# Kernel tuning notes

Hardware: AMD Instinct MI355X
Metric: run time of the kernel (lower is better)

## Reference

```python
import jax, jax.numpy as jnp
import numpy as np
import math

N = 50000
E = 600000
HID = 128
NG = 50
NF = 128
CUTOFF = 10.0
OFFSET = 0.0


def ssp(x):
    # shifted softplus, standard SchNet activation
    return jax.nn.softplus(x) - jnp.log(2.0).astype(x.dtype)


def setup_inputs() -> dict:
    key = jax.random.key(0)
    ks = jax.random.split(key, 12)
    x = jax.random.normal(ks[0], (N, HID), dtype=jnp.float32)
    ji_pairs = jax.random.randint(ks[1], (2, E), 0, N, dtype=jnp.int64)
    e_ji = jax.random.uniform(ks[2], (E,), dtype=jnp.float32) * CUTOFF
    e_ji_basis = jax.random.normal(ks[3], (E, NG), dtype=jnp.float32)
    # filter_nn: Linear(NG, NF) -> ssp -> Linear(NF, NF)
    fw1 = jax.random.normal(ks[4], (NF, NG), dtype=jnp.float32) * (1.0 / np.sqrt(NG))
    fb1 = jnp.zeros((NF,), jnp.float32)
    fw2 = jax.random.normal(ks[5], (NF, NF), dtype=jnp.float32) * (1.0 / np.sqrt(NF))
    fb2 = jnp.zeros((NF,), jnp.float32)
    # CFConv linear1 (no bias), linear2
    w1 = jax.random.normal(ks[6], (NF, HID), dtype=jnp.float32) * (1.0 / np.sqrt(HID))
    w2 = jax.random.normal(ks[7], (HID, NF), dtype=jnp.float32) * (1.0 / np.sqrt(NF))
    b2 = jnp.zeros((HID,), jnp.float32)
    # InteractionBlock linear3
    w3 = jax.random.normal(ks[8], (HID, HID), dtype=jnp.float32) * (1.0 / np.sqrt(HID))
    b3 = jnp.zeros((HID,), jnp.float32)
    return {"x": x, "ji_pairs": ji_pairs, "e_ji": e_ji, "e_ji_basis": e_ji_basis,
            "fw1": fw1, "fb1": fb1, "fw2": fw2, "fb2": fb2,
            "w1": w1, "w2": w2, "b2": b2, "w3": w3, "b3": b3}


def reference(x, ji_pairs, e_ji, e_ji_basis, fw1, fb1, fw2, fb2, w1, w2, b2, w3, b3):
    # cosine cutoff  [E]
    C = 0.25 * (jnp.cos((e_ji - OFFSET) * (np.pi / (CUTOFF - OFFSET))) + 1.0)
    # filter MLP on edge basis  [E, NF]
    h = ssp(e_ji_basis @ fw1.T + fb1)
    W = (h @ fw2.T + fb2) * C[:, None]
    # node projection  [N, NF]
    xh = x @ w1.T
    # gather x_j, modulate by W, scatter-add to target nodes (PyG source_to_target)
    src, dst = ji_pairs[0], ji_pairs[1]
    msg = xh[src] * W                                # [E, NF]
    agg = jax.ops.segment_sum(msg, dst, num_segments=N)  # [N, NF]
    out = agg @ w2.T + b2                            # [N, HID]
    out = ssp(out)
    out = out @ w3.T + b3
    return out
```

## Files before the change

kernel.cpp:

```cpp
#include <hip/hip_runtime.h>

typedef float f32x4 __attribute__((ext_vector_type(4)));
typedef short bf16x8 __attribute__((ext_vector_type(8)));
typedef unsigned short u16;
typedef unsigned int u32;

__device__ __forceinline__ u32 cvt_pk_bf16(float lo, float hi) {
    u32 r;
    asm("v_cvt_pk_bf16_f32 %0, %1, %2" : "=v"(r) : "v"(lo), "v"(hi));
    return r;
}

__device__ __forceinline__ u16 f2b(float f) {
    union { float f; u32 u; } v; v.f = f;
    u32 r = v.u + 0x7fffu + ((v.u >> 16) & 1u);
    return (u16)(r >> 16);
}
__device__ __forceinline__ float b2f_lo(u32 p) {
    union { u32 u; float f; } v; v.u = p << 16; return v.f;
}
__device__ __forceinline__ float b2f_hi(u32 p) {
    union { u32 u; float f; } v; v.u = p & 0xffff0000u; return v.f;
}

__device__ __forceinline__ float ssp(float x) {
    return fmaxf(x, 0.0f) + __logf(1.0f + __expf(-fabsf(x))) - 0.6931471805599453f;
}

__global__ void prep_weights(const float* __restrict__ fw1,
                             const float* __restrict__ fw2,
                             const float* __restrict__ w1,
                             const float* __restrict__ w2,
                             const float* __restrict__ w3,
                             u16* __restrict__ out) {
    int t = blockIdx.x * blockDim.x + threadIdx.x;
    if (t < 128 * 64) {
        int c = t >> 6, k = t & 63;
        out[t] = f2b(k < 50 ? fw1[c * 50 + k] : 0.0f);
        return;
    }
    t -= 128 * 64;
    if (t < 16384) { out[8192 + t] = f2b(fw2[t]); return; }
    t -= 16384;
    if (t < 16384) { out[8192 + 16384 + t] = f2b(w1[t]); return; }
    t -= 16384;
    if (t < 16384) { out[8192 + 32768 + t] = f2b(w2[t]); return; }
    t -= 16384;
    if (t < 16384) { out[8192 + 49152 + t] = f2b(w3[t]); return; }
}

template <int ACT, int OBF>
__global__ __launch_bounds__(256, 3) void linear128(
    const float* __restrict__ in, const u16* __restrict__ wb,
    const float* __restrict__ bias, void* __restrict__ outv, int M) {
    __shared__ u16 in_lds[64 * 136];
    __shared__ u16 w_lds[128 * 136];

    const int tid = threadIdx.x;
    const int r0 = blockIdx.x * 64;

    for (int idx = tid; idx < 128 * 16; idx += 256) {
        int c = idx >> 4, kc = (idx & 15) * 8;
        *reinterpret_cast<uint4*>(&w_lds[c * 136 + kc]) =
            *reinterpret_cast<const uint4*>(&wb[c * 128 + kc]);
    }
    for (int idx = tid; idx < 64 * 32; idx += 256) {
        int r = idx >> 5, kc = (idx & 31) * 4;
        int row = r0 + r;
        float4 v = make_float4(0.f, 0.f, 0.f, 0.f);
        if (row < M) v = *reinterpret_cast<const float4*>(&in[(size_t)row * 128 + kc]);
        u32* p = reinterpret_cast<u32*>(&in_lds[r * 136 + kc]);
        p[0] = cvt_pk_bf16(v.x, v.y); p[1] = cvt_pk_bf16(v.z, v.w);
    }
    __syncthreads();

    const int l = tid & 63, w = tid >> 6;
    const int lr = l & 15, lg = l >> 4;

    f32x4 acc[8] = {};
    for (int ks = 0; ks < 4; ++ks) {
        bf16x8 a = *reinterpret_cast<const bf16x8*>(
            &in_lds[(w * 16 + lr) * 136 + ks * 32 + lg * 8]);
        for (int n = 0; n < 8; ++n) {
            bf16x8 b = *reinterpret_cast<const bf16x8*>(
                &w_lds[(n * 16 + lr) * 136 + ks * 32 + lg * 8]);
            acc[n] = __builtin_amdgcn_mfma_f32_16x16x32_bf16(a, b, acc[n], 0, 0, 0);
        }
    }

    for (int n = 0; n < 8; ++n) {
        int c = n * 16 + lr;
        float bv = bias ? bias[c] : 0.0f;
        for (int i = 0; i < 4; ++i) {
            int row = r0 + w * 16 + lg * 4 + i;
            if (row < M) {
                float v = acc[n][i] + bv;
                if (ACT) v = ssp(v);
                if (OBF) ((u16*)outv)[(size_t)row * 128 + c] = f2b(v);
                else     ((float*)outv)[(size_t)row * 128 + c] = v;
            }
        }
    }
}

__global__ __launch_bounds__(256) void edge_mlp(
    const float* __restrict__ basis, const float* __restrict__ e_ji,
    const u16* __restrict__ fw1b, const u16* __restrict__ fw2b,
    const float* __restrict__ fb1, const float* __restrict__ fb2,
    const int* __restrict__ epos, u16* __restrict__ Wb,
    int E, int nTiles) {
    __shared__ u16 bas[2][32 * 72];
    __shared__ u16 hb[32 * 136];

    const int tid = threadIdx.x;
    const int l = tid & 63, w = tid >> 6;
    const int lr = l & 15, lg = l >> 4;
    const int c8 = lg * 8, c4 = lg * 4;

    bf16x8 wa1[2][2], wa2[2][4];
    float4 b1v[2], b2v[2];
#pragma unroll
    for (int i = 0; i < 2; ++i) {
        const u16* p1 = &fw1b[(size_t)((w * 2 + i) * 16 + lr) * 64];
#pragma unroll
        for (int ks = 0; ks < 2; ++ks)
            wa1[i][ks] = *reinterpret_cast<const bf16x8*>(p1 + ks * 32 + c8);
        const u16* p2 = &fw2b[(size_t)((w * 2 + i) * 16 + lr) * 128];
#pragma unroll
        for (int ks = 0; ks < 4; ++ks)
            wa2[i][ks] = *reinterpret_cast<const bf16x8*>(p2 + ks * 32 + c8);
        b1v[i] = *reinterpret_cast<const float4*>(&fb1[(w * 2 + i) * 16 + c4]);
        b2v[i] = *reinterpret_cast<const float4*>(&fb2[(w * 2 + i) * 16 + c4]);
    }

    for (int idx = tid; idx < 2 * 32 * 7; idx += 256) {
        int b = idx / 224, rem = idx - b * 224;
        int row = rem / 7, q = rem - row * 7;
        *reinterpret_cast<u32*>(&bas[b][row * 72 + 50 + 2 * q]) = 0u;
    }

    int srow[4], scol[4]; bool sv[4];
#pragma unroll
    for (int r = 0; r < 4; ++r) {
        int idx = tid + r * 256;
        sv[r] = idx < 800;
        int rr = idx / 25;
        srow[r] = rr; scol[r] = (idx - rr * 25) * 2;
    }

    int it = blockIdx.x;
    if (it >= nTiles) return;

    float2 stg[4];
#pragma unroll
    for (int r = 0; r < 4; ++r) {
        if (sv[r]) {
            int er = it * 32 + srow[r]; if (er >= E) er = E - 1;
            stg[r] = *reinterpret_cast<const float2*>(&basis[(size_t)er * 50 + scol[r]]);
        }
    }
#pragma unroll
    for (int r = 0; r < 4; ++r)
        if (sv[r])
            *reinterpret_cast<u32*>(&bas[0][srow[r] * 72 + scol[r]]) =
                cvt_pk_bf16(stg[r].x, stg[r].y);

    const int stride = gridDim.x;
    int buf = 0;
    for (; it < nTiles; it += stride) {
        const int nxt = it + stride;
        const bool hn = nxt < nTiles;
        float2 stg2[4];
        if (hn) {
#pragma unroll
            for (int r = 0; r < 4; ++r) {
                if (sv[r]) {
                    int er = nxt * 32 + srow[r]; if (er >= E) er = E - 1;
                    stg2[r] = *reinterpret_cast<const float2*>(
                        &basis[(size_t)er * 50 + scol[r]]);
                }
            }
        }
        const int er0 = it * 32 + lr, er1 = er0 + 16;
        const int ec0 = er0 < E ? er0 : E - 1;
        const int ec1 = er1 < E ? er1 : E - 1;
        const int ep0 = epos[ec0], ep1 = epos[ec1];
        const float ej0 = e_ji[ec0], ej1 = e_ji[ec1];

        __syncthreads();

        f32x4 acc1[2][2] = {};
#pragma unroll
        for (int ks = 0; ks < 2; ++ks) {
            bf16x8 bb0 = *reinterpret_cast<const bf16x8*>(
                &bas[buf][lr * 72 + ks * 32 + c8]);
            bf16x8 bb1 = *reinterpret_cast<const bf16x8*>(
                &bas[buf][(16 + lr) * 72 + ks * 32 + c8]);
#pragma unroll
            for (int i = 0; i < 2; ++i) {
                acc1[0][i] = __builtin_amdgcn_mfma_f32_16x16x32_bf16(wa1[i][ks], bb0, acc1[0][i], 0, 0, 0);
                acc1[1][i] = __builtin_amdgcn_mfma_f32_16x16x32_bf16(wa1[i][ks], bb1, acc1[1][i], 0, 0, 0);
            }
        }
#pragma unroll
        for (int t = 0; t < 2; ++t) {
#pragma unroll
            for (int i = 0; i < 2; ++i) {
                u32* d = reinterpret_cast<u32*>(
                    &hb[(t * 16 + lr) * 136 + (w * 2 + i) * 16 + c4]);
                d[0] = cvt_pk_bf16(ssp(acc1[t][i][0] + b1v[i].x),
                                   ssp(acc1[t][i][1] + b1v[i].y));
                d[1] = cvt_pk_bf16(ssp(acc1[t][i][2] + b1v[i].z),
                                   ssp(acc1[t][i][3] + b1v[i].w));
            }
        }
        __syncthreads();

        f32x4 acc2[2][2] = {};
#pragma unroll
        for (int ks = 0; ks < 4; ++ks) {
            bf16x8 hb0 = *reinterpret_cast<const bf16x8*>(
                &hb[lr * 136 + ks * 32 + c8]);
            bf16x8 hb1 = *reinterpret_cast<const bf16x8*>(
                &hb[(16 + lr) * 136 + ks * 32 + c8]);
#pragma unroll
            for (int i = 0; i < 2; ++i) {
                acc2[0][i] = __builtin_amdgcn_mfma_f32_16x16x32_bf16(wa2[i][ks], hb0, acc2[0][i], 0, 0, 0);
                acc2[1][i] = __builtin_amdgcn_mfma_f32_16x16x32_bf16(wa2[i][ks], hb1, acc2[1][i], 0, 0, 0);
            }
        }
#pragma unroll
        for (int t = 0; t < 2; ++t) {
            const int er = t == 0 ? er0 : er1;
            if (er < E) {
                const float ej = t == 0 ? ej0 : ej1;
                const int pos = t == 0 ? ep0 : ep1;
                const float cv = 0.25f * (__cosf(ej * 0.31415926535897932f) + 1.0f);
#pragma unroll
                for (int i = 0; i < 2; ++i) {
                    uint2 pk;
                    pk.x = cvt_pk_bf16((acc2[t][i][0] + b2v[i].x) * cv,
                                       (acc2[t][i][1] + b2v[i].y) * cv);
                    pk.y = cvt_pk_bf16((acc2[t][i][2] + b2v[i].z) * cv,
                                       (acc2[t][i][3] + b2v[i].w) * cv);
                    *reinterpret_cast<uint2*>(
                        &Wb[(size_t)pos * 128 + (w * 2 + i) * 16 + c4]) = pk;
                }
            }
        }
        if (hn) {
#pragma unroll
            for (int r = 0; r < 4; ++r)
                if (sv[r])
                    *reinterpret_cast<u32*>(&bas[buf ^ 1][srow[r] * 72 + scol[r]]) =
                        cvt_pk_bf16(stg2[r].x, stg2[r].y);
        }
        buf ^= 1;
    }
}

__global__ void hist_kernel(const int* __restrict__ pairs, int* __restrict__ deg, int E) {
    int e = blockIdx.x * blockDim.x + threadIdx.x;
    if (e < E) atomicAdd(&deg[pairs[E + e]], 1);
}

__global__ void scan_a(const int* __restrict__ deg, int* __restrict__ incl,
                       int* __restrict__ bsum, int N) {
    __shared__ int s[256];
    int i = blockIdx.x * 256 + threadIdx.x;
    int v = (i < N) ? deg[i] : 0;
    s[threadIdx.x] = v; __syncthreads();
    for (int off = 1; off < 256; off <<= 1) {
        int t = (threadIdx.x >= off) ? s[threadIdx.x - off] : 0;
        __syncthreads();
        s[threadIdx.x] += t; __syncthreads();
    }
    if (i < N) incl[i] = s[threadIdx.x];
    if (threadIdx.x == 255) bsum[blockIdx.x] = s[255];
}

__global__ void scan_b(int* __restrict__ bsum, int nb) {
    __shared__ int s[256];
    int v = (threadIdx.x < nb) ? bsum[threadIdx.x] : 0;
    s[threadIdx.x] = v; __syncthreads();
    for (int off = 1; off < 256; off <<= 1) {
        int t = (threadIdx.x >= off) ? s[threadIdx.x - off] : 0;
        __syncthreads();
        s[threadIdx.x] += t; __syncthreads();
    }
    if (threadIdx.x < nb) bsum[threadIdx.x] = s[threadIdx.x] - v;
}

__global__ void scan_c(const int* __restrict__ incl, const int* __restrict__ deg,
                       const int* __restrict__ bsum, int* __restrict__ rowst,
                       int* __restrict__ cursor, int N) {
    int i = blockIdx.x * 256 + threadIdx.x;
    if (i < N) {
        int r = incl[i] - deg[i] + bsum[blockIdx.x];
        rowst[i] = r; cursor[i] = r;
    }
}

__global__ void fill_kernel(const int* __restrict__ pairs, int* __restrict__ cursor,
                            int* __restrict__ esrc, int* __restrict__ epos, int E) {
    int e = blockIdx.x * blockDim.x + threadIdx.x;
    if (e < E) {
        int s = pairs[e], d = pairs[E + e];
        int pos = atomicAdd(&cursor[d], 1);
        esrc[pos] = s;
        epos[e] = pos;
    }
}

__global__ __launch_bounds__(256) void aggregate(
    const u16* __restrict__ Wb, const u16* __restrict__ xhb,
    const int* __restrict__ rowst, const int* __restrict__ deg,
    const int* __restrict__ esrc, float* __restrict__ agg, int N) {
    const int w = threadIdx.x >> 6, lane = threadIdx.x & 63;
    const int n = blockIdx.x * 4 + w;
    if (n >= N) return;
    const int rs = rowst[n], d = deg[n];
    float a0 = 0.f, a1 = 0.f;
    int s = (d > 0) ? esrc[rs] : 0;
    for (int k = 0; k < d; ++k) {
        int cur = s;
        if (k + 1 < d) s = esrc[rs + k + 1];
        u32 wp = *reinterpret_cast<const u32*>(&Wb[(size_t)(rs + k) * 128 + lane * 2]);
        u32 xp = *reinterpret_cast<const u32*>(&xhb[(size_t)cur * 128 + lane * 2]);
        a0 = fmaf(b2f_lo(xp), b2f_lo(wp), a0);
        a1 = fmaf(b2f_hi(xp), b2f_hi(wp), a1);
    }
    float2 r; r.x = a0; r.y = a1;
    *reinterpret_cast<float2*>(&agg[(size_t)n * 128 + lane * 2]) = r;
}

__global__ __launch_bounds__(256, 2) void edge_kernel(
    const float* __restrict__ basis, const float* __restrict__ e_ji,
    const int* __restrict__ pairs, const float* __restrict__ xh,
    const u16* __restrict__ fw1b, const u16* __restrict__ fw2b,
    const float* __restrict__ fb1, const float* __restrict__ fb2,
    float* __restrict__ agg, int E) {
    __shared__ u16 hb[64 * 136];
    __shared__ u16 fw1_lds[128 * 72];
    __shared__ u16 fw2_lds[128 * 136];
    __shared__ float cc[64];
    __shared__ int s_src[64];
    __shared__ int s_dst[64];

    const int tid = threadIdx.x;
    const int e0 = blockIdx.x * 64;

    for (int idx = tid; idx < 128 * 8; idx += 256) {
        int c = idx >> 3, kc = (idx & 7) * 8;
        *reinterpret_cast<uint4*>(&fw1_lds[c * 72 + kc]) =
            *reinterpret_cast<const uint4*>(&fw1b[c * 64 + kc]);
    }
    for (int idx = tid; idx < 128 * 16; idx += 256) {
        int c = idx >> 4, kc = (idx & 15) * 8;
        *reinterpret_cast<uint4*>(&fw2_lds[c * 136 + kc]) =
            *reinterpret_cast<const uint4*>(&fw2b[c * 128 + kc]);
    }
    for (int idx = tid; idx < 64 * 64; idx += 256) {
        int e = idx >> 6, k = idx & 63;
        int eg = e0 + e;
        float v = (k < 50 && eg < E) ? basis[(size_t)eg * 50 + k] : 0.0f;
        hb[e * 72 + k] = f2b(v);
    }
    if (tid < 64) {
        int eg = e0 + tid;
        if (eg < E) {
            cc[tid] = 0.25f * (__cosf(e_ji[eg] * 0.31415926535897932f) + 1.0f);
            s_src[tid] = pairs[eg];
            s_dst[tid] = pairs[E + eg];
        } else { cc[tid] = 0.0f; s_src[tid] = 0; s_dst[tid] = 0; }
    }
    __syncthreads();

    const int l = tid & 63, w = tid >> 6;
    const int lr = l & 15, lg = l >> 4;

    f32x4 acc1[8] = {};
    for (int ks = 0; ks < 2; ++ks) {
        bf16x8 a = *reinterpret_cast<const bf16x8*>(
            &hb[(w * 16 + lr) * 72 + ks * 32 + lg * 8]);
        for (int n = 0; n < 8; ++n) {
            bf16x8 b = *reinterpret_cast<const bf16x8*>(
                &fw1_lds[(n * 16 + lr) * 72 + ks * 32 + lg * 8]);
            acc1[n] = __builtin_amdgcn_mfma_f32_16x16x32_bf16(a, b, acc1[n], 0, 0, 0);
        }
    }
    __syncthreads();

    for (int n = 0; n < 8; ++n) {
        int c = n * 16 + lr;
        float bv = fb1[c];
        for (int i = 0; i < 4; ++i) {
            int r = w * 16 + lg * 4 + i;
            hb[r * 136 + c] = f2b(ssp(acc1[n][i] + bv));
        }
    }
    __syncthreads();

    f32x4 acc2[8] = {};
    for (int ks = 0; ks < 4; ++ks) {
        bf16x8 a = *reinterpret_cast<const bf16x8*>(
            &hb[(w * 16 + lr) * 136 + ks * 32 + lg * 8]);
        for (int n = 0; n < 8; ++n) {
            bf16x8 b = *reinterpret_cast<const bf16x8*>(
                &fw2_lds[(n * 16 + lr) * 136 + ks * 32 + lg * 8]);
            acc2[n] = __builtin_amdgcn_mfma_f32_16x16x32_bf16(a, b, acc2[n], 0, 0, 0);
        }
    }

    for (int n = 0; n < 8; ++n) {
        int c = n * 16 + lr;
        float bv = fb2[c];
        for (int i = 0; i < 4; ++i) {
            int eloc = w * 16 + lg * 4 + i;
            if (e0 + eloc < E) {
                float Wv = (acc2[n][i] + bv) * cc[eloc];
                float val = xh[(size_t)s_src[eloc] * 128 + c] * Wv;
                unsafeAtomicAdd(&agg[(size_t)s_dst[eloc] * 128 + c], val);
            }
        }
    }
}

extern "C" void kernel_launch(void* const* d_in, const int* in_sizes, int n_in,
                              void* d_out, int out_size, void* d_ws, size_t ws_size,
                              hipStream_t stream) {
    const float* x      = (const float*)d_in[0];
    const int*   pairs  = (const int*)d_in[1];
    const float* e_ji   = (const float*)d_in[2];
    const float* basis  = (const float*)d_in[3];
    const float* fw1    = (const float*)d_in[4];
    const float* fb1    = (const float*)d_in[5];
    const float* fw2    = (const float*)d_in[6];
    const float* fb2    = (const float*)d_in[7];
    const float* w1     = (const float*)d_in[8];
    const float* w2     = (const float*)d_in[9];
    const float* b2     = (const float*)d_in[10];
    const float* w3     = (const float*)d_in[11];
    const float* b3     = (const float*)d_in[12];
    float* out = (float*)d_out;

    const int N = in_sizes[0] / 128;
    const int E = in_sizes[2];
    const int nodeBlocks = (N + 63) / 64;
    const int nchunks = (N + 255) / 256;
    char* ws = (char*)d_ws;

    size_t off = 0;
    auto nxt = [&](size_t bytes) {
        size_t o = off; off = (off + bytes + 255) & ~(size_t)255; return o;
    };
    u16*   Wb     = (u16*)  (ws + nxt((size_t)E * 128 * 2));
    u16*   xhb    = (u16*)  (ws + nxt((size_t)N * 128 * 2));
    float* agg    = (float*)(ws + nxt((size_t)N * 128 * 4));
    u16*   wb     = (u16*)  (ws + nxt(81920 * 2));
    int*   deg    = (int*)  (ws + nxt((size_t)N * 4));
    int*   incl   = (int*)  (ws + nxt((size_t)N * 4));
    int*   rowst  = (int*)  (ws + nxt((size_t)N * 4));
    int*   cursor = (int*)  (ws + nxt((size_t)N * 4));
    int*   bsum   = (int*)  (ws + nxt(1024));
    int*   esrc   = (int*)  (ws + nxt((size_t)E * 4));
    int*   epos   = (int*)  (ws + nxt((size_t)E * 4));
    const size_t needed = off;

    const u16* fw1b = wb;
    const u16* fw2b = wb + 8192;
    const u16* w1b  = wb + 8192 + 16384;
    const u16* w2b  = wb + 8192 + 32768;
    const u16* w3b  = wb + 8192 + 49152;

    if (ws_size >= needed && nchunks <= 256) {
        prep_weights<<<288, 256, 0, stream>>>(fw1, fw2, w1, w2, w3, wb);
        hipMemsetAsync(deg, 0, (size_t)N * 4, stream);

        linear128<0, 1><<<nodeBlocks, 256, 0, stream>>>(x, w1b, nullptr, xhb, N);

        hist_kernel<<<(E + 255) / 256, 256, 0, stream>>>(pairs, deg, E);
        scan_a<<<nchunks, 256, 0, stream>>>(deg, incl, bsum, N);
        scan_b<<<1, 256, 0, stream>>>(bsum, nchunks);
        scan_c<<<nchunks, 256, 0, stream>>>(incl, deg, bsum, rowst, cursor, N);
        fill_kernel<<<(E + 255) / 256, 256, 0, stream>>>(pairs, cursor, esrc, epos, E);

        const int nTiles = (E + 31) / 32;
        const int grid = nTiles < 2048 ? nTiles : 2048;
        edge_mlp<<<grid, 256, 0, stream>>>(basis, e_ji, fw1b, fw2b,
                                           fb1, fb2, epos, Wb, E, nTiles);
        aggregate<<<(N + 3) / 4, 256, 0, stream>>>(Wb, xhb, rowst, deg,
                                                   esrc, agg, N);

        linear128<1, 0><<<nodeBlocks, 256, 0, stream>>>(agg, w2b, b2, out, N);
        linear128<0, 0><<<nodeBlocks, 256, 0, stream>>>(out, w3b, b3, out, N);
    } else {
        const size_t nodeBytes = (size_t)N * 128 * sizeof(float);
        float* xhf   = (float*)ws;
        float* aggf  = (float*)(ws + nodeBytes);
        u16*   wbf   = (u16*)(ws + 2 * nodeBytes);
        const u16* ffw1b = wbf;
        const u16* ffw2b = wbf + 8192;
        const u16* fw1bw = wbf + 8192 + 16384;
        const u16* fw2bw = wbf + 8192 + 32768;
        const u16* fw3bw = wbf + 8192 + 49152;

        prep_weights<<<288, 256, 0, stream>>>(fw1, fw2, w1, w2, w3, wbf);
        hipMemsetAsync(aggf, 0, nodeBytes, stream);
        linear128<0, 0><<<nodeBlocks, 256, 0, stream>>>(x, fw1bw, nullptr, xhf, N);
        edge_kernel<<<(E + 63) / 64, 256, 0, stream>>>(basis, e_ji, pairs, xhf,
                                                       ffw1b, ffw2b, fb1, fb2, aggf, E);
        linear128<1, 0><<<nodeBlocks, 256, 0, stream>>>(aggf, fw2bw, b2, out, N);
        linear128<0, 0><<<nodeBlocks, 256, 0, stream>>>(out, fw3bw, b3, out, N);
    }
}
```

Before: 326.5 us.

## Fuse tail linears into one kernel, double-buffer edge MLP LDS, deepen aggregate prefetch

Replaces the two node-level linear128 launches (linear2 with ssp, then linear3) with one persistent fused_tail kernel. It keeps the ssp intermediate in LDS, so the N x 128 float intermediate no longer makes a round trip through global memory. In edge_mlp it double-buffers the hidden LDS tile, drops one barrier per iteration, simplifies the basis staging map, and cuts the grid from 2048 to 1536. The aggregate loop now prefetches the next edge's Wb and xh values one step ahead to hide gather latency. The trade-off is more LDS and registers per block.

```diff
diff --git a/kernel.cpp b/kernel.cpp
--- a/kernel.cpp
+++ b/kernel.cpp
@@ -108,9 +108,9 @@
     const u16* __restrict__ fw1b, const u16* __restrict__ fw2b,
     const float* __restrict__ fb1, const float* __restrict__ fb2,
     const int* __restrict__ epos, u16* __restrict__ Wb,
-    int E, int nTiles) {
+    int E, int nTiles, int stride) {
     __shared__ u16 bas[2][32 * 72];
-    __shared__ u16 hb[32 * 136];
+    __shared__ u16 hb[2][32 * 136];
 
     const int tid = threadIdx.x;
     const int l = tid & 63, w = tid >> 6;
@@ -139,46 +139,38 @@
         *reinterpret_cast<u32*>(&bas[b][row * 72 + 50 + 2 * q]) = 0u;
     }
 
-    int srow[4], scol[4]; bool sv[4];
-#pragma unroll
-    for (int r = 0; r < 4; ++r) {
-        int idx = tid + r * 256;
-        sv[r] = idx < 800;
-        int rr = idx / 25;
-        srow[r] = rr; scol[r] = (idx - rr * 25) * 2;
-    }
+    const int srow = tid & 31, cb = tid >> 5;
 
     int it = blockIdx.x;
     if (it >= nTiles) return;
 
-    float2 stg[4];
-#pragma unroll
-    for (int r = 0; r < 4; ++r) {
-        if (sv[r]) {
-            int er = it * 32 + srow[r]; if (er >= E) er = E - 1;
-            stg[r] = *reinterpret_cast<const float2*>(&basis[(size_t)er * 50 + scol[r]]);
-        }
-    }
-#pragma unroll
-    for (int r = 0; r < 4; ++r)
-        if (sv[r])
-            *reinterpret_cast<u32*>(&bas[0][srow[r] * 72 + scol[r]]) =
-                cvt_pk_bf16(stg[r].x, stg[r].y);
-
-    const int stride = gridDim.x;
+    {
+        int er = it * 32 + srow; if (er >= E) er = E - 1;
+        const float* rp = &basis[(size_t)er * 50];
+#pragma unroll
+        for (int r = 0; r < 4; ++r) {
+            int c = cb + r * 8;
+            if (c < 25) {
+                float2 v = *reinterpret_cast<const float2*>(rp + 2 * c);
+                *reinterpret_cast<u32*>(&bas[0][srow * 72 + 2 * c]) =
+                    cvt_pk_bf16(v.x, v.y);
+            }
+        }
+    }
+    __syncthreads();
+
     int buf = 0;
-    for (; it < nTiles; it += stride) {
+    for (; it < nTiles; it += stride, buf ^= 1) {
         const int nxt = it + stride;
         const bool hn = nxt < nTiles;
-        float2 stg2[4];
+        float2 stg[4];
         if (hn) {
+            int er = nxt * 32 + srow; if (er >= E) er = E - 1;
+            const float* rp = &basis[(size_t)er * 50];
 #pragma unroll
             for (int r = 0; r < 4; ++r) {
-                if (sv[r]) {
-                    int er = nxt * 32 + srow[r]; if (er >= E) er = E - 1;
-                    stg2[r] = *reinterpret_cast<const float2*>(
-                        &basis[(size_t)er * 50 + scol[r]]);
-                }
+                int c = cb + r * 8;
+                if (c < 25) stg[r] = *reinterpret_cast<const float2*>(rp + 2 * c);
             }
         }
         const int er0 = it * 32 + lr, er1 = er0 + 16;
@@ -187,8 +179,6 @@
         const int ep0 = epos[ec0], ep1 = epos[ec1];
         const float ej0 = e_ji[ec0], ej1 = e_ji[ec1];
 
-        __syncthreads();
-
         f32x4 acc1[2][2] = {};
 #pragma unroll
         for (int ks = 0; ks < 2; ++ks) {
@@ -207,22 +197,31 @@
 #pragma unroll
             for (int i = 0; i < 2; ++i) {
                 u32* d = reinterpret_cast<u32*>(
-                    &hb[(t * 16 + lr) * 136 + (w * 2 + i) * 16 + c4]);
+                    &hb[buf][(t * 16 + lr) * 136 + (w * 2 + i) * 16 + c4]);
                 d[0] = cvt_pk_bf16(ssp(acc1[t][i][0] + b1v[i].x),
                                    ssp(acc1[t][i][1] + b1v[i].y));
                 d[1] = cvt_pk_bf16(ssp(acc1[t][i][2] + b1v[i].z),
                                    ssp(acc1[t][i][3] + b1v[i].w));
             }
         }
+        if (hn) {
+#pragma unroll
+            for (int r = 0; r < 4; ++r) {
+                int c = cb + r * 8;
+                if (c < 25)
+                    *reinterpret_cast<u32*>(&bas[buf ^ 1][srow * 72 + 2 * c]) =
+                        cvt_pk_bf16(stg[r].x, stg[r].y);
+            }
+        }
         __syncthreads();
 
         f32x4 acc2[2][2] = {};
 #pragma unroll
         for (int ks = 0; ks < 4; ++ks) {
             bf16x8 hb0 = *reinterpret_cast<const bf16x8*>(
-                &hb[lr * 136 + ks * 32 + c8]);
+                &hb[buf][lr * 136 + ks * 32 + c8]);
             bf16x8 hb1 = *reinterpret_cast<const bf16x8*>(
-                &hb[(16 + lr) * 136 + ks * 32 + c8]);
+                &hb[buf][(16 + lr) * 136 + ks * 32 + c8]);
 #pragma unroll
             for (int i = 0; i < 2; ++i) {
                 acc2[0][i] = __builtin_amdgcn_mfma_f32_16x16x32_bf16(wa2[i][ks], hb0, acc2[0][i], 0, 0, 0);
@@ -248,14 +247,130 @@
                 }
             }
         }
+    }
+}
+
+__global__ __launch_bounds__(256) void fused_tail(
+    const float* __restrict__ agg, const u16* __restrict__ w2b,
+    const u16* __restrict__ w3b, const float* __restrict__ b2,
+    const float* __restrict__ b3, float* __restrict__ out,
+    int N, int nTiles, int stride) {
+    __shared__ u16 bas[2][32 * 136];
+    __shared__ u16 hb[2][32 * 136];
+
+    const int tid = threadIdx.x;
+    const int l = tid & 63, w = tid >> 6;
+    const int lr = l & 15, lg = l >> 4;
+    const int c8 = lg * 8, c4 = lg * 4;
+
+    bf16x8 wA[2][4], wB[2][4];
+    float4 b2v[2], b3v[2];
+#pragma unroll
+    for (int i = 0; i < 2; ++i) {
+        const u16* pA = &w2b[(size_t)((w * 2 + i) * 16 + lr) * 128];
+        const u16* pB = &w3b[(size_t)((w * 2 + i) * 16 + lr) * 128];
+#pragma unroll
+        for (int ks = 0; ks < 4; ++ks) {
+            wA[i][ks] = *reinterpret_cast<const bf16x8*>(pA + ks * 32 + c8);
+            wB[i][ks] = *reinterpret_cast<const bf16x8*>(pB + ks * 32 + c8);
+        }
+        b2v[i] = *reinterpret_cast<const float4*>(&b2[(w * 2 + i) * 16 + c4]);
+        b3v[i] = *reinterpret_cast<const float4*>(&b3[(w * 2 + i) * 16 + c4]);
+    }
+
+    const int srow = tid & 31, cb = tid >> 5;
+
+    int it = blockIdx.x;
+    if (it >= nTiles) return;
+
+    {
+        int nd = it * 32 + srow; if (nd >= N) nd = N - 1;
+        const float* rp = &agg[(size_t)nd * 128];
+#pragma unroll
+        for (int r = 0; r < 8; ++r) {
+            int c = cb + r * 8;
+            float2 v = *reinterpret_cast<const float2*>(rp + 2 * c);
+            *reinterpret_cast<u32*>(&bas[0][srow * 136 + 2 * c]) =
+                cvt_pk_bf16(v.x, v.y);
+        }
+    }
+    __syncthreads();
+
+    int buf = 0;
+    for (; it < nTiles; it += stride, buf ^= 1) {
+        const int nxt = it + stride;
+        const bool hn = nxt < nTiles;
+        float2 stg[8];
         if (hn) {
-#pragma unroll
-            for (int r = 0; r < 4; ++r)
-                if (sv[r])
-                    *reinterpret_cast<u32*>(&bas[buf ^ 1][srow[r] * 72 + scol[r]]) =
-                        cvt_pk_bf16(stg2[r].x, stg2[r].y);
-        }
-        buf ^= 1;
+            int nd = nxt * 32 + srow; if (nd >= N) nd = N - 1;
+            const float* rp = &agg[(size_t)nd * 128];
+#pragma unroll
+            for (int r = 0; r < 8; ++r)
+                stg[r] = *reinterpret_cast<const float2*>(rp + 2 * (cb + r * 8));
+        }
+
+        f32x4 acc1[2][2] = {};
+#pragma unroll
+        for (int ks = 0; ks < 4; ++ks) {
+            bf16x8 bb0 = *reinterpret_cast<const bf16x8*>(
+                &bas[buf][lr * 136 + ks * 32 + c8]);
+            bf16x8 bb1 = *reinterpret_cast<const bf16x8*>(
+                &bas[buf][(16 + lr) * 136 + ks * 32 + c8]);
+#pragma unroll
+            for (int i = 0; i < 2; ++i) {
+                acc1[0][i] = __builtin_amdgcn_mfma_f32_16x16x32_bf16(wA[i][ks], bb0, acc1[0][i], 0, 0, 0);
+                acc1[1][i] = __builtin_amdgcn_mfma_f32_16x16x32_bf16(wA[i][ks], bb1, acc1[1][i], 0, 0, 0);
+            }
+        }
+#pragma unroll
+        for (int t = 0; t < 2; ++t) {
+#pragma unroll
+            for (int i = 0; i < 2; ++i) {
+                u32* d = reinterpret_cast<u32*>(
+                    &hb[buf][(t * 16 + lr) * 136 + (w * 2 + i) * 16 + c4]);
+                d[0] = cvt_pk_bf16(ssp(acc1[t][i][0] + b2v[i].x),
+                                   ssp(acc1[t][i][1] + b2v[i].y));
+                d[1] = cvt_pk_bf16(ssp(acc1[t][i][2] + b2v[i].z),
+                                   ssp(acc1[t][i][3] + b2v[i].w));
+            }
+        }
+        if (hn) {
+#pragma unroll
+            for (int r = 0; r < 8; ++r)
+                *reinterpret_cast<u32*>(&bas[buf ^ 1][srow * 136 + 2 * (cb + r * 8)]) =
+                    cvt_pk_bf16(stg[r].x, stg[r].y);
+        }
+        __syncthreads();
+
+        f32x4 acc2[2][2] = {};
+#pragma unroll
+        for (int ks = 0; ks < 4; ++ks) {
+            bf16x8 hb0 = *reinterpret_cast<const bf16x8*>(
+                &hb[buf][lr * 136 + ks * 32 + c8]);
+            bf16x8 hb1 = *reinterpret_cast<const bf16x8*>(
+                &hb[buf][(16 + lr) * 136 + ks * 32 + c8]);
+#pragma unroll
+            for (int i = 0; i < 2; ++i) {
+                acc2[0][i] = __builtin_amdgcn_mfma_f32_16x16x32_bf16(wB[i][ks], hb0, acc2[0][i], 0, 0, 0);
+                acc2[1][i] = __builtin_amdgcn_mfma_f32_16x16x32_bf16(wB[i][ks], hb1, acc2[1][i], 0, 0, 0);
+            }
+        }
+#pragma unroll
+        for (int t = 0; t < 2; ++t) {
+            int nd = it * 32 + t * 16 + lr;
+            if (nd < N) {
+#pragma unroll
+                for (int i = 0; i < 2; ++i) {
+                    float4 o;
+                    o.x = acc2[t][i][0] + b3v[i].x;
+                    o.y = acc2[t][i][1] + b3v[i].y;
+                    o.z = acc2[t][i][2] + b3v[i].z;
+                    o.w = acc2[t][i][3] + b3v[i].w;
+                    *reinterpret_cast<float4*>(
+                        &out[(size_t)nd * 128 + (w * 2 + i) * 16 + c4]) = o;
+                }
+            }
+        }
     }
 }
 
@@ -321,12 +436,20 @@
     if (n >= N) return;
     const int rs = rowst[n], d = deg[n];
     float a0 = 0.f, a1 = 0.f;
-    int s = (d > 0) ? esrc[rs] : 0;
+    int s1 = (d > 0) ? esrc[rs] : 0;
+    int s2 = (d > 1) ? esrc[rs + 1] : 0;
+    u32 wp1 = 0, xp1 = 0;
+    if (d > 0) {
+        wp1 = *reinterpret_cast<const u32*>(&Wb[(size_t)rs * 128 + lane * 2]);
+        xp1 = *reinterpret_cast<const u32*>(&xhb[(size_t)s1 * 128 + lane * 2]);
+    }
     for (int k = 0; k < d; ++k) {
-        int cur = s;
-        if (k + 1 < d) s = esrc[rs + k + 1];
-        u32 wp = *reinterpret_cast<const u32*>(&Wb[(size_t)(rs + k) * 128 + lane * 2]);
-        u32 xp = *reinterpret_cast<const u32*>(&xhb[(size_t)cur * 128 + lane * 2]);
+        u32 wp = wp1, xp = xp1;
+        if (k + 1 < d) {
+            wp1 = *reinterpret_cast<const u32*>(&Wb[(size_t)(rs + k + 1) * 128 + lane * 2]);
+            xp1 = *reinterpret_cast<const u32*>(&xhb[(size_t)s2 * 128 + lane * 2]);
+        }
+        if (k + 2 < d) s2 = esrc[rs + k + 2];
         a0 = fmaf(b2f_lo(xp), b2f_lo(wp), a0);
         a1 = fmaf(b2f_hi(xp), b2f_hi(wp), a1);
     }
@@ -486,14 +609,16 @@
         fill_kernel<<<(E + 255) / 256, 256, 0, stream>>>(pairs, cursor, esrc, epos, E);
 
         const int nTiles = (E + 31) / 32;
-        const int grid = nTiles < 2048 ? nTiles : 2048;
-        edge_mlp<<<grid, 256, 0, stream>>>(basis, e_ji, fw1b, fw2b,
-                                           fb1, fb2, epos, Wb, E, nTiles);
+        const int gridE = nTiles < 1536 ? nTiles : 1536;
+        edge_mlp<<<gridE, 256, 0, stream>>>(basis, e_ji, fw1b, fw2b,
+                                            fb1, fb2, epos, Wb, E, nTiles, gridE);
         aggregate<<<(N + 3) / 4, 256, 0, stream>>>(Wb, xhb, rowst, deg,
                                                    esrc, agg, N);
 
-        linear128<1, 0><<<nodeBlocks, 256, 0, stream>>>(agg, w2b, b2, out, N);
-        linear128<0, 0><<<nodeBlocks, 256, 0, stream>>>(out, w3b, b3, out, N);
+        const int ntT = (N + 31) / 32;
+        const int gridT = ntT < 1024 ? ntT : 1024;
+        fused_tail<<<gridT, 256, 0, stream>>>(agg, w2b, w3b, b2, b3, out,
+                                              N, ntT, gridT);
     } else {
         const size_t nodeBytes = (size_t)N * 128 * sizeof(float);
         float* xhf   = (float*)ws;
```

Result: faster. 303.7 us (-7.0%).
